# Kernel optimization log

Measured on AMD Instinct MI355X. Metric: run time of the kernel, lower is better.

The kernel has to match this reference:

```python
import jax, jax.numpy as jnp
import numpy as np

BLANK = 0

def setup_inputs() -> dict:
    key = jax.random.key(0)
    # [B, T, Num_labels] CTC logits
    emission = jax.random.normal(key, (64, 8192, 32), dtype=jnp.float32)
    return {"emission": emission}

def reference(emission):
    # Greedy best path: argmax over labels -> [B, T]
    idx = jnp.argmax(emission, axis=-1).astype(jnp.int32)
    B, T = idx.shape
    # torch.unique_consecutive(indices, dim=-1) on a [B,T] tensor drops a
    # COLUMN t iff the entire column equals column t-1 (slice-wise dedup).
    col_keep = jnp.concatenate([
        jnp.ones((1,), dtype=bool),
        jnp.any(idx[:, 1:] != idx[:, :-1], axis=0),
    ])  # [T]
    # Per-row blank filtering of the surviving columns (the python loop in torch).
    keep = col_keep[None, :] & (idx != BLANK)  # [B, T]
    lens = jnp.sum(keep, axis=-1).astype(jnp.int32)  # [B]
    # Stream compaction via prefix-sum: kept tokens move left, rest -> overflow col.
    pos = jnp.cumsum(keep.astype(jnp.int32), axis=-1) - 1  # [B, T]
    pos = jnp.where(keep, pos, T)  # masked-out entries go to column T (dropped)
    rows = jnp.broadcast_to(jnp.arange(B)[:, None], (B, T))
    btokens = jnp.full((B, T + 1), BLANK, dtype=jnp.int32)
    btokens = btokens.at[rows, pos].set(idx)[:, :T]  # blank-padded to T (static shape)
    return (btokens, lens)
```

## Files before the change

### kernel.cpp

```cpp
#include <hip/hip_runtime.h>
#include <hip/hip_bf16.h>

#define CTC_B 64
#define CTC_T 8192
#define CTC_V 32
#define BLANK 0

typedef float f32x4 __attribute__((ext_vector_type(4)));

__global__ __launch_bounds__(256) void ctc_argmax_kernel(
    const float* __restrict__ em, unsigned char* __restrict__ idx) {
    const int tid = blockIdx.x * blockDim.x + threadIdx.x;
    const int g   = tid >> 2;
    const int sub = tid & 3;

    const f32x4* base = reinterpret_cast<const f32x4*>(em);
    const f32x4* pa = base + ((size_t)(2 * g)    ) * 8 + sub;
    const f32x4* pb = base + ((size_t)(2 * g) + 1) * 8 + sub;
    f32x4 a0 = __builtin_nontemporal_load(pa);
    f32x4 a1 = __builtin_nontemporal_load(pa + 4);
    f32x4 b0 = __builtin_nontemporal_load(pb);
    f32x4 b1 = __builtin_nontemporal_load(pb + 4);

    const int i1 = sub * 4, i2 = 16 + sub * 4;

    float bA = a0.x; int iA = i1;
    if (a0.y > bA) { bA = a0.y; iA = i1 + 1; }
    if (a0.z > bA) { bA = a0.z; iA = i1 + 2; }
    if (a0.w > bA) { bA = a0.w; iA = i1 + 3; }
    if (a1.x > bA) { bA = a1.x; iA = i2;     }
    if (a1.y > bA) { bA = a1.y; iA = i2 + 1; }
    if (a1.z > bA) { bA = a1.z; iA = i2 + 2; }
    if (a1.w > bA) { bA = a1.w; iA = i2 + 3; }

    float bB = b0.x; int iB = i1;
    if (b0.y > bB) { bB = b0.y; iB = i1 + 1; }
    if (b0.z > bB) { bB = b0.z; iB = i1 + 2; }
    if (b0.w > bB) { bB = b0.w; iB = i1 + 3; }
    if (b1.x > bB) { bB = b1.x; iB = i2;     }
    if (b1.y > bB) { bB = b1.y; iB = i2 + 1; }
    if (b1.z > bB) { bB = b1.z; iB = i2 + 2; }
    if (b1.w > bB) { bB = b1.w; iB = i2 + 3; }

#pragma unroll
    for (int m = 1; m < 4; m <<= 1) {
        float oA = __shfl_xor(bA, m, 64);
        int   jA = __shfl_xor(iA, m, 64);
        float oB = __shfl_xor(bB, m, 64);
        int   jB = __shfl_xor(iB, m, 64);
        if (oA > bA || (oA == bA && jA < iA)) { bA = oA; iA = jA; }
        if (oB > bB || (oB == bB && jB < iB)) { bB = oB; iB = jB; }
    }
    if (sub == 0) {
        unsigned short pk = (unsigned short)((iA & 0xff) | ((iB & 0xff) << 8));
        *reinterpret_cast<unsigned short*>(idx + 2 * g) = pk;
    }
}

__device__ __forceinline__ unsigned long long nzmask(unsigned long long x) {
    return (x | ((x & 0x7f7f7f7f7f7f7f7fULL) + 0x7f7f7f7f7f7f7f7fULL))
           & 0x8080808080808080ULL;
}

__global__ __launch_bounds__(1024) void ctc_compact_kernel(
    const unsigned char* __restrict__ idx,
    int* __restrict__ btokens, int* __restrict__ lens) {
    const int b   = blockIdx.x;
    const int tid = threadIdx.x;
    const int t8  = tid * 8;
    const unsigned char* row = idx + (size_t)b * CTC_T;
    int* orow = btokens + (size_t)b * CTC_T;

    __shared__ int s_wsum[16];
    const int lane = tid & 63;
    const int wid  = tid >> 6;

    const unsigned long long xv = *reinterpret_cast<const unsigned long long*>(row + t8);
    const unsigned char* r0 = idx;
    const unsigned char* r1 = idx + CTC_T;
    unsigned long long x0 = *reinterpret_cast<const unsigned long long*>(r0 + t8);
    unsigned long long x1 = *reinterpret_cast<const unsigned long long*>(r1 + t8);
    unsigned char p0 = (t8 == 0) ? (unsigned char)0 : r0[t8 - 1];
    unsigned char p1 = (t8 == 0) ? (unsigned char)0 : r1[t8 - 1];

    unsigned long long hk = nzmask(x0 ^ ((x0 << 8) | (unsigned long long)p0))
                          | nzmask(x1 ^ ((x1 << 8) | (unsigned long long)p1));
    if (t8 == 0) hk |= 0x80ULL;

    unsigned long long und = ~hk & 0x8080808080808080ULL;
    for (int bb = 2; bb < CTC_B && und; ++bb) {
        const unsigned char* rb = idx + (size_t)bb * CTC_T;
        unsigned long long xb = *reinterpret_cast<const unsigned long long*>(rb + t8);
        unsigned char pb = (t8 == 0) ? (unsigned char)0 : rb[t8 - 1];
        hk |= nzmask(xb ^ ((xb << 8) | (unsigned long long)pb));
        und = ~hk & 0x8080808080808080ULL;
    }

    const unsigned long long keep_hi = hk & nzmask(xv);
    const int c = __popcll(keep_hi);

    int scan = c;
#pragma unroll
    for (int m = 1; m < 64; m <<= 1) {
        int o = __shfl_up(scan, m, 64);
        if (lane >= m) scan += o;
    }
    if (lane == 63) s_wsum[wid] = scan;
    __syncthreads();

    int woff = 0, total = 0;
#pragma unroll
    for (int w = 0; w < 16; ++w) {
        int x = s_wsum[w];
        if (w < wid) woff += x;
        total += x;
    }
    int pos = woff + (scan - c);

#pragma unroll
    for (int j = 0; j < 8; ++j) {
        if (keep_hi & (0x80ULL << (8 * j))) {
            orow[pos++] = (int)((xv >> (8 * j)) & 0xffULL);
        }
    }

    int vstart = (total + 3) & ~3;
    if (tid < vstart - total) orow[total + tid] = BLANK;
    int4* vout = reinterpret_cast<int4*>(orow + vstart);
    const int nvec = (CTC_T - vstart) >> 2;
    const int4 z = make_int4(BLANK, BLANK, BLANK, BLANK);
    for (int i = tid; i < nvec; i += 1024) vout[i] = z;
    if (tid == 0) lens[b] = total;
}

extern "C" void kernel_launch(void* const* d_in, const int* in_sizes, int n_in,
                              void* d_out, int out_size, void* d_ws, size_t ws_size,
                              hipStream_t stream) {
    const float* emission = (const float*)d_in[0];
    int* out = (int*)d_out;
    int* btokens = out;
    int* lens = out + (size_t)CTC_B * CTC_T;

    unsigned char* idx = (unsigned char*)d_ws;

    const int total_threads = CTC_B * CTC_T * 2;
    ctc_argmax_kernel<<<total_threads / 256, 256, 0, stream>>>(emission, idx);
    ctc_compact_kernel<<<CTC_B, 1024, 0, stream>>>(idx, btokens, lens);
}
```

Baseline: 21.65 us.

## Fuse argmax and compaction into one cooperative persistent kernel with grid sync

Replaces the two launches (argmax, then per-row compaction) with a single cooperative kernel of 256 blocks × 1024 threads. Each thread loops over several argmax units, the whole grid synchronises, and the first 64 blocks then do the compaction. The aim is to remove the second launch and its gap. In exchange it adds a grid-wide barrier, lowers occupancy in the argmax phase, and leaves most blocks idle during compaction.

```diff
diff --git a/kernel.cpp b/kernel.cpp
--- a/kernel.cpp
+++ b/kernel.cpp
@@ -1,71 +1,87 @@
 #include <hip/hip_runtime.h>
 #include <hip/hip_bf16.h>
+#include <hip/hip_cooperative_groups.h>
+
+namespace cg = cooperative_groups;
 
 #define CTC_B 64
 #define CTC_T 8192
 #define CTC_V 32
 #define BLANK 0
 
+#define BLOCKS 256
+#define TPB 1024
+#define UNITS (CTC_B * CTC_T / 2)
+#define GROUPS_PER_PASS (BLOCKS * TPB / 4)
+#define K_ITERS (UNITS / GROUPS_PER_PASS)
+
 typedef float f32x4 __attribute__((ext_vector_type(4)));
-
-__global__ __launch_bounds__(256) void ctc_argmax_kernel(
-    const float* __restrict__ em, unsigned char* __restrict__ idx) {
-    const int tid = blockIdx.x * blockDim.x + threadIdx.x;
-    const int g   = tid >> 2;
-    const int sub = tid & 3;
-
-    const f32x4* base = reinterpret_cast<const f32x4*>(em);
-    const f32x4* pa = base + ((size_t)(2 * g)    ) * 8 + sub;
-    const f32x4* pb = base + ((size_t)(2 * g) + 1) * 8 + sub;
-    f32x4 a0 = __builtin_nontemporal_load(pa);
-    f32x4 a1 = __builtin_nontemporal_load(pa + 4);
-    f32x4 b0 = __builtin_nontemporal_load(pb);
-    f32x4 b1 = __builtin_nontemporal_load(pb + 4);
-
-    const int i1 = sub * 4, i2 = 16 + sub * 4;
-
-    float bA = a0.x; int iA = i1;
-    if (a0.y > bA) { bA = a0.y; iA = i1 + 1; }
-    if (a0.z > bA) { bA = a0.z; iA = i1 + 2; }
-    if (a0.w > bA) { bA = a0.w; iA = i1 + 3; }
-    if (a1.x > bA) { bA = a1.x; iA = i2;     }
-    if (a1.y > bA) { bA = a1.y; iA = i2 + 1; }
-    if (a1.z > bA) { bA = a1.z; iA = i2 + 2; }
-    if (a1.w > bA) { bA = a1.w; iA = i2 + 3; }
-
-    float bB = b0.x; int iB = i1;
-    if (b0.y > bB) { bB = b0.y; iB = i1 + 1; }
-    if (b0.z > bB) { bB = b0.z; iB = i1 + 2; }
-    if (b0.w > bB) { bB = b0.w; iB = i1 + 3; }
-    if (b1.x > bB) { bB = b1.x; iB = i2;     }
-    if (b1.y > bB) { bB = b1.y; iB = i2 + 1; }
-    if (b1.z > bB) { bB = b1.z; iB = i2 + 2; }
-    if (b1.w > bB) { bB = b1.w; iB = i2 + 3; }
-
-#pragma unroll
-    for (int m = 1; m < 4; m <<= 1) {
-        float oA = __shfl_xor(bA, m, 64);
-        int   jA = __shfl_xor(iA, m, 64);
-        float oB = __shfl_xor(bB, m, 64);
-        int   jB = __shfl_xor(iB, m, 64);
-        if (oA > bA || (oA == bA && jA < iA)) { bA = oA; iA = jA; }
-        if (oB > bB || (oB == bB && jB < iB)) { bB = oB; iB = jB; }
-    }
-    if (sub == 0) {
-        unsigned short pk = (unsigned short)((iA & 0xff) | ((iB & 0xff) << 8));
-        *reinterpret_cast<unsigned short*>(idx + 2 * g) = pk;
-    }
-}
 
 __device__ __forceinline__ unsigned long long nzmask(unsigned long long x) {
     return (x | ((x & 0x7f7f7f7f7f7f7f7fULL) + 0x7f7f7f7f7f7f7f7fULL))
            & 0x8080808080808080ULL;
 }
 
-__global__ __launch_bounds__(1024) void ctc_compact_kernel(
-    const unsigned char* __restrict__ idx,
+__global__ __launch_bounds__(TPB) void ctc_fused_kernel(
+    const float* __restrict__ em, unsigned char* __restrict__ idx,
     int* __restrict__ btokens, int* __restrict__ lens) {
-    const int b   = blockIdx.x;
+
+    {
+        const int tid = blockIdx.x * TPB + threadIdx.x;
+        const int g0  = tid >> 2;
+        const int sub = tid & 3;
+        const int i1 = sub * 4, i2 = 16 + sub * 4;
+        const f32x4* base = reinterpret_cast<const f32x4*>(em);
+
+#pragma unroll
+        for (int k = 0; k < K_ITERS; ++k) {
+            const int u = g0 + k * GROUPS_PER_PASS;
+            const f32x4* pa = base + ((size_t)u * 16) + sub;
+            f32x4 a0 = __builtin_nontemporal_load(pa);
+            f32x4 a1 = __builtin_nontemporal_load(pa + 4);
+            f32x4 b0 = __builtin_nontemporal_load(pa + 8);
+            f32x4 b1 = __builtin_nontemporal_load(pa + 12);
+
+            float bA = a0.x; int iA = i1;
+            if (a0.y > bA) { bA = a0.y; iA = i1 + 1; }
+            if (a0.z > bA) { bA = a0.z; iA = i1 + 2; }
+            if (a0.w > bA) { bA = a0.w; iA = i1 + 3; }
+            if (a1.x > bA) { bA = a1.x; iA = i2;     }
+            if (a1.y > bA) { bA = a1.y; iA = i2 + 1; }
+            if (a1.z > bA) { bA = a1.z; iA = i2 + 2; }
+            if (a1.w > bA) { bA = a1.w; iA = i2 + 3; }
+
+            float bB = b0.x; int iB = i1;
+            if (b0.y > bB) { bB = b0.y; iB = i1 + 1; }
+            if (b0.z > bB) { bB = b0.z; iB = i1 + 2; }
+            if (b0.w > bB) { bB = b0.w; iB = i1 + 3; }
+            if (b1.x > bB) { bB = b1.x; iB = i2;     }
+            if (b1.y > bB) { bB = b1.y; iB = i2 + 1; }
+            if (b1.z > bB) { bB = b1.z; iB = i2 + 2; }
+            if (b1.w > bB) { bB = b1.w; iB = i2 + 3; }
+
+#pragma unroll
+            for (int m = 1; m < 4; m <<= 1) {
+                float oA = __shfl_xor(bA, m, 64);
+                int   jA = __shfl_xor(iA, m, 64);
+                float oB = __shfl_xor(bB, m, 64);
+                int   jB = __shfl_xor(iB, m, 64);
+                if (oA > bA || (oA == bA && jA < iA)) { bA = oA; iA = jA; }
+                if (oB > bB || (oB == bB && jB < iB)) { bB = oB; iB = jB; }
+            }
+            if (sub == 0) {
+                unsigned short pk =
+                    (unsigned short)((iA & 0xff) | ((iB & 0xff) << 8));
+                *reinterpret_cast<unsigned short*>(idx + 2 * (size_t)u) = pk;
+            }
+        }
+    }
+
+    cg::this_grid().sync();
+
+    const int b = blockIdx.x;
+    if (b >= CTC_B) return;
+
     const int tid = threadIdx.x;
     const int t8  = tid * 8;
     const unsigned char* row = idx + (size_t)b * CTC_T;
@@ -129,7 +145,7 @@
     int4* vout = reinterpret_cast<int4*>(orow + vstart);
     const int nvec = (CTC_T - vstart) >> 2;
     const int4 z = make_int4(BLANK, BLANK, BLANK, BLANK);
-    for (int i = tid; i < nvec; i += 1024) vout[i] = z;
+    for (int i = tid; i < nvec; i += TPB) vout[i] = z;
     if (tid == 0) lens[b] = total;
 }
 
@@ -140,10 +156,9 @@
     int* out = (int*)d_out;
     int* btokens = out;
     int* lens = out + (size_t)CTC_B * CTC_T;
-
     unsigned char* idx = (unsigned char*)d_ws;
 
-    const int total_threads = CTC_B * CTC_T * 2;
-    ctc_argmax_kernel<<<total_threads / 256, 256, 0, stream>>>(emission, idx);
-    ctc_compact_kernel<<<CTC_B, 1024, 0, stream>>>(idx, btokens, lens);
+    void* args[] = {(void*)&emission, (void*)&idx, (void*)&btokens, (void*)&lens};
+    hipLaunchCooperativeKernel((const void*)ctc_fused_kernel,
+                               dim3(BLOCKS), dim3(TPB), args, 0, stream);
 }
```

New measurement: 58.08 us. +168.2%, slower.
